# Kernel optimization log

Measured on AMD Instinct MI355X. Metric: run time of the kernel, lower is better.

Reference implementation:

```python
import jax, jax.numpy as jnp
import numpy as np
from jax import lax

NUM_GROUP = 512
GROUP_SIZE = 32


def fps(xyz, npoint):
    """Farthest point sampling. xyz: [B, N, 3] -> centers [B, npoint, 3]."""
    B, N, _ = xyz.shape
    big = jnp.asarray(1e10, xyz.dtype)

    def body(carry, _):
        min_d, farthest = carry  # [B, N], [B]
        centroid = jnp.take_along_axis(xyz, farthest[:, None, None], axis=1)  # [B,1,3]
        d = jnp.sum((xyz - centroid) ** 2, axis=-1)  # [B, N]
        min_d = jnp.minimum(min_d, d)
        nxt = jnp.argmax(min_d, axis=-1).astype(jnp.int32)
        return (min_d, nxt), farthest

    init = (jnp.full((B, N), big, xyz.dtype), jnp.zeros((B,), jnp.int32))
    _, idxs = lax.scan(body, init, None, length=npoint)  # [npoint, B]
    idxs = idxs.T  # [B, npoint]
    return jnp.take_along_axis(xyz, idxs[..., None], axis=1)  # [B, npoint, 3]


def knn_idx(xyz, center, k):
    """xyz [B,N,3], center [B,G,3] -> idx [B,G,k] of k nearest (squared L2)."""
    # [B, G, N] squared distances
    d2 = jnp.sum((center[:, :, None, :] - xyz[:, None, :, :]) ** 2, axis=-1)
    _, idx = lax.top_k(-d2, k)  # smallest distances
    return idx


def setup_inputs() -> dict:
    key = jax.random.key(0)
    xyz = jax.random.normal(key, (32, 3, 8192), dtype=jnp.float32)
    return {"xyz": xyz}


def reference(xyz):
    # xyz: [B, 3, N] -> [B, N, 3]
    pts = jnp.transpose(xyz, (0, 2, 1))[:, :, :3]
    B, N, _ = pts.shape
    center = fps(pts, NUM_GROUP)                  # [B, G, 3]
    idx = knn_idx(pts, center, GROUP_SIZE)        # [B, G, k]
    flat_idx = idx.reshape(B, NUM_GROUP * GROUP_SIZE)
    neighborhood = jnp.take_along_axis(pts, flat_idx[..., None], axis=1)
    neighborhood = neighborhood.reshape(B, NUM_GROUP, GROUP_SIZE, 3)
    neighborhood = neighborhood - center[:, :, None, :]
    return neighborhood, center
```

## Files before the change

### kernel.cpp

```cpp
#include <hip/hip_runtime.h>

typedef unsigned long long u64;
typedef unsigned int u32;

#define BATCH 32
#define NPTS  8192
#define NGRP  512
#define KNN_K 32

#define FPS_T 512
#define FPS_W (FPS_T / 64)
#define PPT   (NPTS / FPS_T)
#define KNN_WPB 4
#define QCAP 128

__device__ __forceinline__ float sq3(float dx, float dy, float dz) {
    return __fadd_rn(__fadd_rn(__fmul_rn(dx, dx), __fmul_rn(dy, dy)), __fmul_rn(dz, dz));
}

__device__ __forceinline__ u64 packdi(float d, int n) {
    return ((u64)__float_as_uint(d) << 32) | (u32)n;
}

__device__ __forceinline__ u64 umin64(u64 a, u64 b) { return a < b ? a : b; }
__device__ __forceinline__ u64 umax64(u64 a, u64 b) { return a > b ? a : b; }

__device__ __forceinline__ u64 shfl_xor_u64(u64 v, int m) {
    int lo = __shfl_xor((int)(u32)v, m, 64);
    int hi = __shfl_xor((int)(u32)(v >> 32), m, 64);
    return ((u64)(u32)hi << 32) | (u32)lo;
}

__device__ __forceinline__ u64 shfl_u64(u64 v, int src) {
    int lo = __shfl((int)(u32)v, src, 64);
    int hi = __shfl((int)(u32)(v >> 32), src, 64);
    return ((u64)(u32)hi << 32) | (u32)lo;
}

template <int CTRL>
__device__ __forceinline__ u64 dpp_max_step(u64 k) {
    u32 plo = (u32)__builtin_amdgcn_update_dpp(0, (int)(u32)k, CTRL, 0xF, 0xF, true);
    u32 phi = (u32)__builtin_amdgcn_update_dpp(0, (int)(u32)(k >> 32), CTRL, 0xF, 0xF, true);
    u64 p = ((u64)phi << 32) | plo;
    return k > p ? k : p;
}
__device__ __forceinline__ u64 dpp_wave_max(u64 k) {
    k = dpp_max_step<0x111>(k);
    k = dpp_max_step<0x112>(k);
    k = dpp_max_step<0x114>(k);
    k = dpp_max_step<0x118>(k);
    k = dpp_max_step<0x142>(k);
    k = dpp_max_step<0x143>(k);
    return k;
}

__device__ __forceinline__ u64 lane_sort64(u64 v, int lane) {
#pragma unroll
    for (int k = 2; k <= 64; k <<= 1) {
#pragma unroll
        for (int j = k >> 1; j > 0; j >>= 1) {
            u64 p = shfl_xor_u64(v, j);
            bool keepmin = (((lane & k) == 0) == ((lane & j) == 0));
            u64 mn = umin64(v, p), mx = umax64(v, p);
            v = keepmin ? mn : mx;
        }
    }
    return v;
}

__device__ __forceinline__ u64 lane_merge64(u64 m, u64 c, int lane) {
    u64 cr = shfl_xor_u64(c, 63);
    u64 z = umin64(m, cr);
#pragma unroll
    for (int dd = 32; dd > 0; dd >>= 1) {
        u64 p = shfl_xor_u64(z, dd);
        u64 mn = umin64(z, p), mx = umax64(z, p);
        z = (lane & dd) ? mx : mn;
    }
    return z;
}

__global__ __launch_bounds__(FPS_T) void fps_kernel(const float* __restrict__ in,
                                                    float* __restrict__ centers) {
    __shared__ float sx[NPTS];
    __shared__ float sy[NPTS];
    __shared__ float sz[NPTS];
    __shared__ u64 s_key[2][FPS_W];
    __shared__ float s_out[NGRP * 3];

    const int b = blockIdx.x;
    const int t = threadIdx.x;
    const int w = t >> 6;
    const float* xp = in + (size_t)b * 3 * NPTS;
    const float* yp = xp + NPTS;
    const float* zp = xp + 2 * NPTS;

    float xr[PPT], yr[PPT], zr[PPT], md[PPT];
#pragma unroll
    for (int i = 0; i < PPT; ++i) {
        int n = i * FPS_T + t;
        float x = xp[n], y = yp[n], z = zp[n];
        xr[i] = x; yr[i] = y; zr[i] = z;
        sx[n] = x; sy[n] = y; sz[n] = z;
        md[i] = 1e10f;
    }
    __syncthreads();

    int cur = 0;
    for (int r = 0; r < NGRP; ++r) {
        const float cx = sx[cur], cy = sy[cur], cz = sz[cur];
        if (t == 0) {
            s_out[r * 3 + 0] = cx;
            s_out[r * 3 + 1] = cy;
            s_out[r * 3 + 2] = cz;
        }

#pragma unroll
        for (int i = 0; i < PPT; ++i) {
            float d = sq3(__fsub_rn(xr[i], cx), __fsub_rn(yr[i], cy), __fsub_rn(zr[i], cz));
            md[i] = fminf(md[i], d);
        }
        float m01 = fmaxf(md[0], md[1]),   m23 = fmaxf(md[2], md[3]);
        float m45 = fmaxf(md[4], md[5]),   m67 = fmaxf(md[6], md[7]);
        float m89 = fmaxf(md[8], md[9]),   mab = fmaxf(md[10], md[11]);
        float mcd = fmaxf(md[12], md[13]), mef = fmaxf(md[14], md[15]);
        float q0 = fmaxf(m01, m23), q1 = fmaxf(m45, m67);
        float q2 = fmaxf(m89, mab), q3 = fmaxf(mcd, mef);
        float mxs = fmaxf(fmaxf(q0, q1), fmaxf(q2, q3));
        int s = 0;
#pragma unroll
        for (int i = PPT - 1; i >= 0; --i) {
            if (md[i] == mxs) s = i;
        }
        int c = s * FPS_T + t;
        u64 k = ((u64)__float_as_uint(mxs) << 32) | (u32)(~(u32)c);
        k = dpp_wave_max(k);
        if ((t & 63) == 63) s_key[r & 1][w] = k;
        __syncthreads();
        u64 m = s_key[r & 1][0];
#pragma unroll
        for (int i = 1; i < FPS_W; ++i) m = umax64(m, s_key[r & 1][i]);
        cur = (int)(~(u32)m);
    }

    __syncthreads();
    float* cdst = centers + (size_t)b * NGRP * 3;
    for (int i = t; i < NGRP * 3; i += FPS_T) cdst[i] = s_out[i];
}

__global__ __launch_bounds__(KNN_WPB * 64) void knn_kernel(const float* __restrict__ in,
                                                           const float* __restrict__ centers,
                                                           float* __restrict__ out) {
    __shared__ u64 sbuf[KNN_WPB][QCAP];

    const int wave = threadIdx.x >> 6;
    const int lane = threadIdx.x & 63;
    const int cid  = blockIdx.x * KNN_WPB + wave;
    const int b    = cid >> 9;

    const float* xp = in + (size_t)b * 3 * NPTS;
    const float* yp = xp + NPTS;
    const float* zp = xp + 2 * NPTS;

    const float cx = centers[cid * 3 + 0];
    const float cy = centers[cid * 3 + 1];
    const float cz = centers[cid * 3 + 2];

    float x = xp[lane], y = yp[lane], z = zp[lane];
    u64 m = packdi(sq3(__fsub_rn(x, cx), __fsub_rn(y, cy), __fsub_rn(z, cz)), lane);
    m = lane_sort64(m, lane);
    u64 tau = shfl_u64(m, 31);
    int cnt = 0;

    float nx = xp[64 + lane], ny = yp[64 + lane], nz = zp[64 + lane];
#pragma unroll 1
    for (int j = 1; j < NPTS / 64; ++j) {
        x = nx; y = ny; z = nz;
        if (j + 1 < NPTS / 64) {
            int n2 = (j + 1) * 64 + lane;
            nx = xp[n2]; ny = yp[n2]; nz = zp[n2];
        }
        float d = sq3(__fsub_rn(x, cx), __fsub_rn(y, cy), __fsub_rn(z, cz));
        u64 kk = packdi(d, j * 64 + lane);
        bool cand = kk < tau;
        u64 mask = __ballot(cand);
        if (mask) {
            u32 below = __builtin_amdgcn_mbcnt_hi(
                (u32)(mask >> 32), __builtin_amdgcn_mbcnt_lo((u32)mask, 0));
            if (cand) sbuf[wave][cnt + below] = kk;
            cnt += (int)__popcll(mask);
            if (cnt >= 64) {
                u64 c = sbuf[wave][lane];
                c = lane_sort64(c, lane);
                m = lane_merge64(m, c, lane);
                tau = shfl_u64(m, 31);
                int rem = cnt - 64;
                if (lane < rem) sbuf[wave][lane] = sbuf[wave][64 + lane];
                cnt = rem;
            }
        }
    }
    while (cnt > 0) {
        int take = cnt < 64 ? cnt : 64;
        u64 v = sbuf[wave][lane];
        u64 c = (lane < take) ? v : ~0ull;
        c = lane_sort64(c, lane);
        m = lane_merge64(m, c, lane);
        int rem = cnt - take;
        if (lane < rem) sbuf[wave][lane] = sbuf[wave][64 + lane];
        cnt = rem;
    }

    if (lane < KNN_K) {
        int n = (int)(u32)m;
        size_t o = (size_t)cid * (KNN_K * 3) + (size_t)lane * 3;
        out[o + 0] = __fsub_rn(xp[n], cx);
        out[o + 1] = __fsub_rn(yp[n], cy);
        out[o + 2] = __fsub_rn(zp[n], cz);
    }
}

extern "C" void kernel_launch(void* const* d_in, const int* in_sizes, int n_in,
                              void* d_out, int out_size, void* d_ws, size_t ws_size,
                              hipStream_t stream) {
    const float* in  = (const float*)d_in[0];
    float* out       = (float*)d_out;
    float* centers   = out + (size_t)BATCH * NGRP * KNN_K * 3;

    fps_kernel<<<BATCH, FPS_T, 0, stream>>>(in, centers);
    knn_kernel<<<(BATCH * NGRP) / KNN_WPB, KNN_WPB * 64, 0, stream>>>(in, centers, out);
}
```

Baseline: 632.2 us.

## Spatially bin FPS points per wave and skip waves via bounding-box bound

The FPS kernel now uses 1024 threads and sorts points into z-slabs, one per wave, using a sigmoid-of-normalized-z bucketing with a shared histogram and scatter. Each wave keeps an axis-aligned bounding box of its points. In each round it computes a lower bound on the distance from the new center to that box. If the bound cannot lower the wave's current max min-distance, the wave skips the distance update and reuses its previous key. Ties are broken by original index stored in a u16 array. This adds setup cost, atomics and branch divergence, and relies on the slabs being balanced for the input distribution.

```diff
diff --git a/kernel.cpp b/kernel.cpp
--- a/kernel.cpp
+++ b/kernel.cpp
@@ -2,13 +2,14 @@
 
 typedef unsigned long long u64;
 typedef unsigned int u32;
+typedef unsigned short u16;
 
 #define BATCH 32
 #define NPTS  8192
 #define NGRP  512
 #define KNN_K 32
 
-#define FPS_T 512
+#define FPS_T 1024
 #define FPS_W (FPS_T / 64)
 #define PPT   (NPTS / FPS_T)
 #define KNN_WPB 4
@@ -80,67 +81,173 @@
     return z;
 }
 
+__device__ __forceinline__ float bf_min(float v) {
+#pragma unroll
+    for (int off = 1; off < 64; off <<= 1) v = fminf(v, __shfl_xor(v, off, 64));
+    return v;
+}
+__device__ __forceinline__ float bf_max(float v) {
+#pragma unroll
+    for (int off = 1; off < 64; off <<= 1) v = fmaxf(v, __shfl_xor(v, off, 64));
+    return v;
+}
+
 __global__ __launch_bounds__(FPS_T) void fps_kernel(const float* __restrict__ in,
                                                     float* __restrict__ centers) {
     __shared__ float sx[NPTS];
     __shared__ float sy[NPTS];
     __shared__ float sz[NPTS];
-    __shared__ u64 s_key[2][FPS_W];
+    __shared__ u16   sidx[NPTS];
+    __shared__ u64   s_key[2][FPS_W];
     __shared__ float s_out[NGRP * 3];
+    __shared__ float s_red[2 * FPS_W];
+    __shared__ float s_stats[2];
+    __shared__ int   s_hist[FPS_W];
+    __shared__ int   s_off[FPS_W];
 
     const int b = blockIdx.x;
     const int t = threadIdx.x;
     const int w = t >> 6;
+    const int lane = t & 63;
     const float* xp = in + (size_t)b * 3 * NPTS;
     const float* yp = xp + NPTS;
     const float* zp = xp + 2 * NPTS;
 
-    float xr[PPT], yr[PPT], zr[PPT], md[PPT];
+    float ztmp[PPT];
+    float zsum = 0.f, zsq = 0.f;
 #pragma unroll
     for (int i = 0; i < PPT; ++i) {
         int n = i * FPS_T + t;
-        float x = xp[n], y = yp[n], z = zp[n];
-        xr[i] = x; yr[i] = y; zr[i] = z;
-        sx[n] = x; sy[n] = y; sz[n] = z;
+        float z = zp[n];
+        ztmp[i] = z;
+        zsum += z;
+        zsq += z * z;
+    }
+#pragma unroll
+    for (int off = 1; off < 64; off <<= 1) {
+        zsum += __shfl_xor(zsum, off, 64);
+        zsq  += __shfl_xor(zsq,  off, 64);
+    }
+    if (lane == 0) { s_red[w] = zsum; s_red[FPS_W + w] = zsq; }
+    if (t < FPS_W) s_hist[t] = 0;
+    __syncthreads();
+    if (t == 0) {
+        float S = 0.f, Q = 0.f;
+        for (int i = 0; i < FPS_W; ++i) { S += s_red[i]; Q += s_red[FPS_W + i]; }
+        float mu = S / (float)NPTS;
+        float var = Q / (float)NPTS - mu * mu;
+        s_stats[0] = mu;
+        s_stats[1] = rsqrtf(fmaxf(var, 1e-12f));
+    }
+    __syncthreads();
+    const float mu = s_stats[0], invs = s_stats[1];
+
+    int slab[PPT];
+#pragma unroll
+    for (int i = 0; i < PPT; ++i) {
+        float u = (ztmp[i] - mu) * invs * 1.702f;
+        float sg = 1.0f / (1.0f + __expf(-u));
+        int sb = (int)(sg * (float)FPS_W);
+        slab[i] = min(FPS_W - 1, max(0, sb));
+        atomicAdd(&s_hist[slab[i]], 1);
+    }
+    __syncthreads();
+    if (t < FPS_W) {
+        int acc = 0;
+        for (int j = 0; j < t; ++j) acc += s_hist[j];
+        s_off[t] = acc;
+    }
+    __syncthreads();
+#pragma unroll
+    for (int i = 0; i < PPT; ++i) {
+        int n = i * FPS_T + t;
+        int pos = atomicAdd(&s_off[slab[i]], 1);
+        sx[pos] = xp[n];
+        sy[pos] = yp[n];
+        sz[pos] = ztmp[i];
+        sidx[pos] = (u16)n;
+    }
+    __syncthreads();
+
+    float xr[PPT], yr[PPT], zr[PPT], md[PPT];
+#pragma unroll
+    for (int i = 0; i < PPT; ++i) {
+        int p = (w << 9) + (i << 6) + lane;
+        xr[i] = sx[p]; yr[i] = sy[p]; zr[i] = sz[p];
         md[i] = 1e10f;
     }
-    __syncthreads();
-
-    int cur = 0;
+    float lx = xr[0], hx = xr[0], ly = yr[0], hy = yr[0], lz = zr[0], hz = zr[0];
+#pragma unroll
+    for (int i = 1; i < PPT; ++i) {
+        lx = fminf(lx, xr[i]); hx = fmaxf(hx, xr[i]);
+        ly = fminf(ly, yr[i]); hy = fmaxf(hy, yr[i]);
+        lz = fminf(lz, zr[i]); hz = fmaxf(hz, zr[i]);
+    }
+    lx = bf_min(lx); hx = bf_max(hx);
+    ly = bf_min(ly); hy = bf_max(hy);
+    lz = bf_min(lz); hz = bf_max(hz);
+
+    float cx = xp[0], cy = yp[0], cz = zp[0];
+    float prev_maxmd = 1e10f;
+    u64 prevkey = 0;
+
     for (int r = 0; r < NGRP; ++r) {
-        const float cx = sx[cur], cy = sy[cur], cz = sz[cur];
         if (t == 0) {
             s_out[r * 3 + 0] = cx;
             s_out[r * 3 + 1] = cy;
             s_out[r * 3 + 2] = cz;
         }
-
-#pragma unroll
-        for (int i = 0; i < PPT; ++i) {
-            float d = sq3(__fsub_rn(xr[i], cx), __fsub_rn(yr[i], cy), __fsub_rn(zr[i], cz));
-            md[i] = fminf(md[i], d);
-        }
-        float m01 = fmaxf(md[0], md[1]),   m23 = fmaxf(md[2], md[3]);
-        float m45 = fmaxf(md[4], md[5]),   m67 = fmaxf(md[6], md[7]);
-        float m89 = fmaxf(md[8], md[9]),   mab = fmaxf(md[10], md[11]);
-        float mcd = fmaxf(md[12], md[13]), mef = fmaxf(md[14], md[15]);
-        float q0 = fmaxf(m01, m23), q1 = fmaxf(m45, m67);
-        float q2 = fmaxf(m89, mab), q3 = fmaxf(mcd, mef);
-        float mxs = fmaxf(fmaxf(q0, q1), fmaxf(q2, q3));
-        int s = 0;
-#pragma unroll
-        for (int i = PPT - 1; i >= 0; --i) {
-            if (md[i] == mxs) s = i;
-        }
-        int c = s * FPS_T + t;
-        u64 k = ((u64)__float_as_uint(mxs) << 32) | (u32)(~(u32)c);
-        k = dpp_wave_max(k);
-        if ((t & 63) == 63) s_key[r & 1][w] = k;
+        float gx = fmaxf(0.f, fmaxf(lx - cx, cx - hx));
+        float gy = fmaxf(0.f, fmaxf(ly - cy, cy - hy));
+        float gz = fmaxf(0.f, fmaxf(lz - cz, cz - hz));
+        float lb = gx * gx + gy * gy + gz * gz;
+        if (lb * 0.99999f < prev_maxmd) {
+#pragma unroll
+            for (int i = 0; i < PPT; ++i) {
+                float d = sq3(__fsub_rn(xr[i], cx), __fsub_rn(yr[i], cy),
+                              __fsub_rn(zr[i], cz));
+                md[i] = fminf(md[i], d);
+            }
+            float m01 = fmaxf(md[0], md[1]), m23 = fmaxf(md[2], md[3]);
+            float m45 = fmaxf(md[4], md[5]), m67 = fmaxf(md[6], md[7]);
+            float mxs = fmaxf(fmaxf(m01, m23), fmaxf(m45, m67));
+            int s = 0, cnt = 0;
+#pragma unroll
+            for (int i = PPT - 1; i >= 0; --i) {
+                bool h = (md[i] == mxs);
+                if (h) s = i;
+                cnt += (int)h;
+            }
+            int p = (w << 9) + (s << 6) + lane;
+            u32 oidx;
+            if (cnt > 1) {
+                oidx = 0xFFFFu;
+#pragma unroll
+                for (int i = 0; i < PPT; ++i) {
+                    if (md[i] == mxs) {
+                        int pp = (w << 9) + (i << 6) + lane;
+                        u32 oi = (u32)sidx[pp];
+                        if (oi < oidx) { oidx = oi; p = pp; }
+                    }
+                }
+            } else {
+                oidx = (u32)sidx[p];
+            }
+            u64 k = ((u64)__float_as_uint(mxs) << 32) |
+                    ((u64)(0xFFFFu ^ oidx) << 16) | (u32)p;
+            k = dpp_wave_max(k);
+            if (lane == 63) s_key[r & 1][w] = k;
+        } else {
+            if (lane == 63) s_key[r & 1][w] = prevkey;
+        }
         __syncthreads();
         u64 m = s_key[r & 1][0];
 #pragma unroll
         for (int i = 1; i < FPS_W; ++i) m = umax64(m, s_key[r & 1][i]);
-        cur = (int)(~(u32)m);
+        prevkey = s_key[r & 1][w];
+        prev_maxmd = __uint_as_float((u32)(prevkey >> 32));
+        int cp = (int)(m & 0xFFFFu);
+        cx = sx[cp]; cy = sy[cp]; cz = sz[cp];
     }
 
     __syncthreads();
```

After: 703.6 us. 1.11x slower.

## Shrink FPS block, forward winner coords via shared memory, batch KNN loads

Applied to the files above, without the earlier changes.

FPS now runs with 256 threads (32 points per thread) and fuses the per-point max and argmax into a single pass. Each wave's winner writes its coordinates to shared memory, so the next center is picked by a branch-free select over four waves instead of a dependent shared-memory lookup after the barrier. This shortens the serial critical path of each of the 512 rounds. The KNN scan now loads 8 chunks of coordinates at once before processing them, giving more memory-level parallelism. The cost is higher register pressure and fewer threads per FPS block.

```diff
diff --git a/kernel.cpp b/kernel.cpp
--- a/kernel.cpp
+++ b/kernel.cpp
@@ -8,7 +8,7 @@
 #define NGRP  512
 #define KNN_K 32
 
-#define FPS_T 512
+#define FPS_T 256
 #define FPS_W (FPS_T / 64)
 #define PPT   (NPTS / FPS_T)
 #define KNN_WPB 4
@@ -80,17 +80,44 @@
     return z;
 }
 
+__device__ __forceinline__ void knn_step(u64& m, u64& tau, int& cnt, u64* sbuf,
+                                         float x, float y, float z,
+                                         float cx, float cy, float cz,
+                                         int n, int lane) {
+    float d = sq3(__fsub_rn(x, cx), __fsub_rn(y, cy), __fsub_rn(z, cz));
+    u64 kk = packdi(d, n);
+    bool cand = kk < tau;
+    u64 mask = __ballot(cand);
+    if (mask) {
+        u32 below = __builtin_amdgcn_mbcnt_hi(
+            (u32)(mask >> 32), __builtin_amdgcn_mbcnt_lo((u32)mask, 0));
+        if (cand) sbuf[cnt + below] = kk;
+        cnt += (int)__popcll(mask);
+        if (cnt >= 64) {
+            u64 c = sbuf[lane];
+            c = lane_sort64(c, lane);
+            m = lane_merge64(m, c, lane);
+            tau = shfl_u64(m, 31);
+            int rem = cnt - 64;
+            if (lane < rem) sbuf[lane] = sbuf[64 + lane];
+            cnt = rem;
+        }
+    }
+}
+
 __global__ __launch_bounds__(FPS_T) void fps_kernel(const float* __restrict__ in,
                                                     float* __restrict__ centers) {
     __shared__ float sx[NPTS];
     __shared__ float sy[NPTS];
     __shared__ float sz[NPTS];
-    __shared__ u64 s_key[2][FPS_W];
+    __shared__ u64   s_key[2][FPS_W];
+    __shared__ float s_wc[2][3][FPS_W];
     __shared__ float s_out[NGRP * 3];
 
     const int b = blockIdx.x;
     const int t = threadIdx.x;
     const int w = t >> 6;
+    const int lane = t & 63;
     const float* xp = in + (size_t)b * 3 * NPTS;
     const float* yp = xp + NPTS;
     const float* zp = xp + 2 * NPTS;
@@ -106,41 +133,52 @@
     }
     __syncthreads();
 
-    int cur = 0;
+    float cx = sx[0], cy = sy[0], cz = sz[0];
+
     for (int r = 0; r < NGRP; ++r) {
-        const float cx = sx[cur], cy = sy[cur], cz = sz[cur];
         if (t == 0) {
             s_out[r * 3 + 0] = cx;
             s_out[r * 3 + 1] = cy;
             s_out[r * 3 + 2] = cz;
         }
 
+        float bd = -1.0f;
+        int   s  = 0;
 #pragma unroll
         for (int i = 0; i < PPT; ++i) {
-            float d = sq3(__fsub_rn(xr[i], cx), __fsub_rn(yr[i], cy), __fsub_rn(zr[i], cz));
+            float d = sq3(__fsub_rn(xr[i], cx), __fsub_rn(yr[i], cy),
+                          __fsub_rn(zr[i], cz));
             md[i] = fminf(md[i], d);
-        }
-        float m01 = fmaxf(md[0], md[1]),   m23 = fmaxf(md[2], md[3]);
-        float m45 = fmaxf(md[4], md[5]),   m67 = fmaxf(md[6], md[7]);
-        float m89 = fmaxf(md[8], md[9]),   mab = fmaxf(md[10], md[11]);
-        float mcd = fmaxf(md[12], md[13]), mef = fmaxf(md[14], md[15]);
-        float q0 = fmaxf(m01, m23), q1 = fmaxf(m45, m67);
-        float q2 = fmaxf(m89, mab), q3 = fmaxf(mcd, mef);
-        float mxs = fmaxf(fmaxf(q0, q1), fmaxf(q2, q3));
-        int s = 0;
-#pragma unroll
-        for (int i = PPT - 1; i >= 0; --i) {
-            if (md[i] == mxs) s = i;
-        }
-        int c = s * FPS_T + t;
-        u64 k = ((u64)__float_as_uint(mxs) << 32) | (u32)(~(u32)c);
+            if (md[i] > bd) { bd = md[i]; s = i; }
+        }
+        const int bi = (s << 8) + t;
+        u64 k = ((u64)__float_as_uint(bd) << 32) | (u32)(~(u32)bi);
         k = dpp_wave_max(k);
-        if ((t & 63) == 63) s_key[r & 1][w] = k;
+        if (lane == 63) {
+            const int nw = (int)(~(u32)k) & (NPTS - 1);
+            const float wx = sx[nw], wy = sy[nw], wz = sz[nw];
+            s_key[r & 1][w] = k;
+            s_wc[r & 1][0][w] = wx;
+            s_wc[r & 1][1][w] = wy;
+            s_wc[r & 1][2][w] = wz;
+        }
         __syncthreads();
-        u64 m = s_key[r & 1][0];
-#pragma unroll
-        for (int i = 1; i < FPS_W; ++i) m = umax64(m, s_key[r & 1][i]);
-        cur = (int)(~(u32)m);
+        const u64 k0 = s_key[r & 1][0], k1 = s_key[r & 1][1];
+        const u64 k2 = s_key[r & 1][2], k3 = s_key[r & 1][3];
+        const float x0 = s_wc[r & 1][0][0], y0 = s_wc[r & 1][1][0], z0 = s_wc[r & 1][2][0];
+        const float x1 = s_wc[r & 1][0][1], y1 = s_wc[r & 1][1][1], z1 = s_wc[r & 1][2][1];
+        const float x2 = s_wc[r & 1][0][2], y2 = s_wc[r & 1][1][2], z2 = s_wc[r & 1][2][2];
+        const float x3 = s_wc[r & 1][0][3], y3 = s_wc[r & 1][1][3], z3 = s_wc[r & 1][2][3];
+        const bool a01 = (k0 >= k1);
+        const u64  m01 = a01 ? k0 : k1;
+        const float xa = a01 ? x0 : x1, ya = a01 ? y0 : y1, za = a01 ? z0 : z1;
+        const bool a23 = (k2 >= k3);
+        const u64  m23 = a23 ? k2 : k3;
+        const float xb = a23 ? x2 : x3, yb = a23 ? y2 : y3, zb = a23 ? z2 : z3;
+        const bool af = (m01 >= m23);
+        cx = af ? xa : xb;
+        cy = af ? ya : yb;
+        cz = af ? za : zb;
     }
 
     __syncthreads();
@@ -172,33 +210,25 @@
     u64 tau = shfl_u64(m, 31);
     int cnt = 0;
 
-    float nx = xp[64 + lane], ny = yp[64 + lane], nz = zp[64 + lane];
+    int j = 1;
 #pragma unroll 1
-    for (int j = 1; j < NPTS / 64; ++j) {
-        x = nx; y = ny; z = nz;
-        if (j + 1 < NPTS / 64) {
-            int n2 = (j + 1) * 64 + lane;
-            nx = xp[n2]; ny = yp[n2]; nz = zp[n2];
-        }
-        float d = sq3(__fsub_rn(x, cx), __fsub_rn(y, cy), __fsub_rn(z, cz));
-        u64 kk = packdi(d, j * 64 + lane);
-        bool cand = kk < tau;
-        u64 mask = __ballot(cand);
-        if (mask) {
-            u32 below = __builtin_amdgcn_mbcnt_hi(
-                (u32)(mask >> 32), __builtin_amdgcn_mbcnt_lo((u32)mask, 0));
-            if (cand) sbuf[wave][cnt + below] = kk;
-            cnt += (int)__popcll(mask);
-            if (cnt >= 64) {
-                u64 c = sbuf[wave][lane];
-                c = lane_sort64(c, lane);
-                m = lane_merge64(m, c, lane);
-                tau = shfl_u64(m, 31);
-                int rem = cnt - 64;
-                if (lane < rem) sbuf[wave][lane] = sbuf[wave][64 + lane];
-                cnt = rem;
-            }
-        }
+    for (; j + 7 < NPTS / 64; j += 8) {
+        int n0 = j * 64 + lane;
+        float xv[8], yv[8], zv[8];
+#pragma unroll
+        for (int q = 0; q < 8; ++q) {
+            xv[q] = xp[n0 + q * 64];
+            yv[q] = yp[n0 + q * 64];
+            zv[q] = zp[n0 + q * 64];
+        }
+#pragma unroll
+        for (int q = 0; q < 8; ++q)
+            knn_step(m, tau, cnt, sbuf[wave], xv[q], yv[q], zv[q],
+                     cx, cy, cz, n0 + q * 64, lane);
+    }
+    for (; j < NPTS / 64; ++j) {
+        int n = j * 64 + lane;
+        knn_step(m, tau, cnt, sbuf[wave], xp[n], yp[n], zp[n], cx, cy, cz, n, lane);
     }
     while (cnt > 0) {
         int take = cnt < 64 ? cnt : 64;
```

Result: no change. 627.4 us (-0.8%).
